# Performance work log

Measured on AMD Instinct MI355X. Metric: run time of the kernel, lower is better.

## Reference

```python
import jax, jax.numpy as jnp
import numpy as np

B, T, S, E = 32, 256, 9, 631     # batch, time, index_len, emb_num
D, FF, H, L, OUT = 512, 512, 8, 2, 512  # d_model, ffn, heads, layers, output_dim
HD = D // H
EPS = 1e-5


def _layernorm(x, g, b):
    m = jnp.mean(x, axis=-1, keepdims=True)
    v = jnp.mean(jnp.square(x - m), axis=-1, keepdims=True)
    return (x - m) * jax.lax.rsqrt(v + EPS) * g + b


def _encoder_layer(h, qkv_w, qkv_b, out_w, out_b, ln1_g, ln1_b,
                   lin1_w, lin1_b, lin2_w, lin2_b, ln2_g, ln2_b):
    # h: (N, S, D). PyTorch post-norm TransformerEncoderLayer, relu activation, dropout=0.
    N = h.shape[0]
    qkv = h @ qkv_w + qkv_b                       # (N, S, 3D)
    q, k, v = jnp.split(qkv, 3, axis=-1)
    q = q.reshape(N, S, H, HD)
    k = k.reshape(N, S, H, HD)
    v = v.reshape(N, S, H, HD)
    scores = jnp.einsum('nqhd,nkhd->nhqk', q, k) / jnp.sqrt(jnp.float32(HD))
    attn = jax.nn.softmax(scores, axis=-1)
    ctx = jnp.einsum('nhqk,nkhd->nqhd', attn, v).reshape(N, S, D)
    h = _layernorm(h + (ctx @ out_w + out_b), ln1_g, ln1_b)
    ff = jax.nn.relu(h @ lin1_w + lin1_b) @ lin2_w + lin2_b
    return _layernorm(h + ff, ln2_g, ln2_b)


def _forward(x, adapt2_w, adapt2_b, adapt_w, adapt_b,
             qkv_w, qkv_b, out_w, out_b, ln1_g, ln1_b,
             lin1_w, lin1_b, lin2_w, lin2_b, ln2_g, ln2_b, fc_w, fc_b):
    # eye_mat[x] @ W^T is a row gather: adapt_layer(onehot) == adapt_w[x] + adapt_b
    emb = adapt_w[x] + adapt_b                               # (B, T, S, D)
    # adapt_ly2(onehot.reshape(B,T,9*E)) == sum_n W2r[n, x[...,n]] + b
    w2r = adapt2_w.reshape(S, E, OUT)
    raw_emb = w2r[jnp.arange(S)[None, None, :], x].sum(axis=2) + adapt2_b  # (B, T, OUT)

    h = emb.reshape(B * T, S, D)
    for l in range(L):
        h = _encoder_layer(h, qkv_w[l], qkv_b[l], out_w[l], out_b[l],
                           ln1_g[l], ln1_b[l], lin1_w[l], lin1_b[l],
                           lin2_w[l], lin2_b[l], ln2_g[l], ln2_b[l])
    cls = h[:, 0, :]                                         # x[0] in seq-first layout
    ov = (cls @ fc_w + fc_b).reshape(B, T, OUT)
    return raw_emb * (1.0 + jax.nn.relu(ov))


def setup_inputs() -> dict:
    key = jax.random.key(0)
    ks = jax.random.split(key, 20)
    s = 0.02
    inp = {
        'x': jax.random.randint(ks[0], (B, T, S), 0, E),
        'adapt2_w': jax.random.normal(ks[1], (S * E, OUT), jnp.float32) * s,
        'adapt2_b': jnp.zeros((OUT,), jnp.float32),
        'adapt_w': jax.random.normal(ks[2], (E, D), jnp.float32) * s,
        'adapt_b': jnp.zeros((D,), jnp.float32),
        'qkv_w': jax.random.normal(ks[3], (L, D, 3 * D), jnp.float32) * s,
        'qkv_b': jnp.zeros((L, 3 * D), jnp.float32),
        'out_w': jax.random.normal(ks[4], (L, D, D), jnp.float32) * s,
        'out_b': jnp.zeros((L, D), jnp.float32),
        'ln1_g': jnp.ones((L, D), jnp.float32),
        'ln1_b': jnp.zeros((L, D), jnp.float32),
        'lin1_w': jax.random.normal(ks[5], (L, D, FF), jnp.float32) * s,
        'lin1_b': jnp.zeros((L, FF), jnp.float32),
        'lin2_w': jax.random.normal(ks[6], (L, FF, D), jnp.float32) * s,
        'lin2_b': jnp.zeros((L, D), jnp.float32),
        'ln2_g': jnp.ones((L, D), jnp.float32),
        'ln2_b': jnp.zeros((L, D), jnp.float32),
        'fc_w': jax.random.normal(ks[7], (D, OUT), jnp.float32) * s,
        'fc_b': jnp.zeros((OUT,), jnp.float32),
    }
    return inp


def reference(x, adapt2_w, adapt2_b, adapt_w, adapt_b, qkv_w, qkv_b, out_w,
              out_b, ln1_g, ln1_b, lin1_w, lin1_b, lin2_w, lin2_b, ln2_g,
              ln2_b, fc_w, fc_b):
    return _forward(x, adapt2_w, adapt2_b, adapt_w, adapt_b, qkv_w, qkv_b,
                    out_w, out_b, ln1_g, ln1_b, lin1_w, lin1_b, lin2_w,
                    lin2_b, ln2_g, ln2_b, fc_w, fc_b)
```

## Files before the change

### kernel.cpp

```cpp
#include <hip/hip_runtime.h>
#include <hip/hip_bf16.h>
#include <stdint.h>

typedef __bf16 bf16;
typedef bf16 bf16x8 __attribute__((ext_vector_type(8)));
typedef bf16 bf16x2 __attribute__((ext_vector_type(2)));
typedef float f32x4 __attribute__((ext_vector_type(4)));

__device__ __forceinline__ float b2f(bf16 x) {
  unsigned short u = __builtin_bit_cast(unsigned short, x);
  unsigned int v = ((unsigned int)u) << 16;
  return __builtin_bit_cast(float, v);
}
__device__ __forceinline__ bf16 f2b(float f) {
  unsigned int u = __builtin_bit_cast(unsigned int, f);
  unsigned int r = (u + 0x7FFFu + ((u >> 16) & 1u)) >> 16;
  return __builtin_bit_cast(bf16, (unsigned short)r);
}

__device__ __forceinline__ void async_copy16(const bf16* g, bf16* l) {
  __builtin_amdgcn_global_load_lds(
      (const __attribute__((address_space(1))) void*)g,
      (__attribute__((address_space(3))) void*)l, 16, 0, 0);
}

template <int MFR, int LDA, int LDC, int RSTR, bool RELU, bool RESID, bool RAWG, bool F32OUT, bool SWZ>
__global__ __launch_bounds__(256, (MFR == 6 ? 3 : 4)) void gemm_kernel(
    const bf16* __restrict__ A,
    const bf16* __restrict__ BT,
    const float* __restrict__ bias,
    const bf16* __restrict__ resid,
    const float* __restrict__ rawg,
    bf16* __restrict__ Cb, float* __restrict__ Cf)
{
  constexpr int K = 512;
  constexpr int MROWS = MFR * 32;
  __shared__ bf16 As[MROWS * 64];
  __shared__ bf16 Bs[128 * 64];
  const int t = threadIdx.x;
  const int lane = t & 63;
  const int wave = t >> 6;

  int bx, by;
  if (SWZ) {
    const int gn = gridDim.x, gm = gridDim.y;
    int id = blockIdx.y * gn + blockIdx.x;
    int full = (gm & ~7) * gn;
    if (id < full) {
      int sg = id / (8 * gn);
      int r = id - sg * (8 * gn);
      by = sg * 8 + (r & 7);
      bx = r >> 3;
    } else {
      int r = id - full;
      int rem = gm - (gm & ~7);
      by = (gm & ~7) + (r % rem);
      bx = r / rem;
    }
  } else {
    bx = blockIdx.x; by = blockIdx.y;
  }

  const long m0 = (long)by * MROWS;
  const int n0 = bx * 128;
  const int wm = (wave >> 1) * (MFR * 16);
  const int wn = (wave & 1) * 64;
  const int row16 = lane & 15;
  const int quad = lane >> 4;

  f32x4 acc[MFR][4] = {};

  const bf16* gA[MFR]; const bf16* gB[4];
  bf16* lA[MFR]; bf16* lB[4];
#pragma unroll
  for (int i = 0; i < MFR; i++) {
    int c = i * 256 + t;
    int row = c >> 3;
    int kc = (c & 7) ^ (row & 7);
    gA[i] = A + (m0 + row) * LDA + kc * 8;
    lA[i] = As + i * 2048 + wave * 512;
  }
#pragma unroll
  for (int i = 0; i < 4; i++) {
    int c = i * 256 + t;
    int row = c >> 3;
    int kc = (c & 7) ^ (row & 7);
    gB[i] = BT + (long)(n0 + row) * K + kc * 8;
    lB[i] = Bs + i * 2048 + wave * 512;
  }

  const int rb7 = row16 & 7;
  const bf16* paA = As + (wm + row16) * 64;
  const bf16* pbB = Bs + (wn + row16) * 64;
  const int o0 = ((0 + quad) ^ rb7) * 8;
  const int o1 = ((4 + quad) ^ rb7) * 8;

#pragma unroll 1
  for (int kt = 0; kt < K; kt += 64) {
#pragma unroll
    for (int i = 0; i < MFR; i++) async_copy16(gA[i] + kt, lA[i]);
#pragma unroll
    for (int i = 0; i < 4; i++) async_copy16(gB[i] + kt, lB[i]);
    __syncthreads();
    {
      bf16x8 af[MFR], bfr[4];
#pragma unroll
      for (int i = 0; i < MFR; i++) af[i] = *(const bf16x8*)(paA + i * 1024 + o0);
#pragma unroll
      for (int i = 0; i < 4; i++) bfr[i] = *(const bf16x8*)(pbB + i * 1024 + o0);
#pragma unroll
      for (int mi = 0; mi < MFR; mi++)
#pragma unroll
        for (int ni = 0; ni < 4; ni++)
          acc[mi][ni] = __builtin_amdgcn_mfma_f32_16x16x32_bf16(af[mi], bfr[ni], acc[mi][ni], 0, 0, 0);
    }
    {
      bf16x8 af[MFR], bfr[4];
#pragma unroll
      for (int i = 0; i < MFR; i++) af[i] = *(const bf16x8*)(paA + i * 1024 + o1);
#pragma unroll
      for (int i = 0; i < 4; i++) bfr[i] = *(const bf16x8*)(pbB + i * 1024 + o1);
#pragma unroll
      for (int mi = 0; mi < MFR; mi++)
#pragma unroll
        for (int ni = 0; ni < 4; ni++)
          acc[mi][ni] = __builtin_amdgcn_mfma_f32_16x16x32_bf16(af[mi], bfr[ni], acc[mi][ni], 0, 0, 0);
    }
    __syncthreads();
  }

  float bv[4];
#pragma unroll
  for (int ni = 0; ni < 4; ni++) bv[ni] = bias[n0 + wn + ni * 16 + row16];
#pragma unroll
  for (int mi = 0; mi < MFR; mi++) {
    long rb = m0 + wm + mi * 16 + quad * 4;
#pragma unroll
    for (int ni = 0; ni < 4; ni++) {
      int col = n0 + wn + ni * 16 + row16;
#pragma unroll
      for (int r = 0; r < 4; r++) {
        float xv = acc[mi][ni][r] + bv[ni];
        if (RESID) xv += b2f(resid[(rb + r) * RSTR + col]);
        if (RELU) xv = fmaxf(xv, 0.f);
        if (RAWG) xv = rawg[(rb + r) * 512 + col] * (1.f + fmaxf(xv, 0.f));
        if (F32OUT) Cf[(rb + r) * LDC + col] = xv;
        else        Cb[(rb + r) * LDC + col] = f2b(xv);
      }
    }
  }
}

#define ROWP 520
__global__ __launch_bounds__(512) void attn_kernel(bf16* __restrict__ qkv)
{
  __shared__ bf16 q[9 * ROWP];
  __shared__ bf16 k[9 * ROWP];
  __shared__ bf16 v[9 * ROWP];
  __shared__ float sc[8 * 81];
  const long n = blockIdx.x;
  const int t = threadIdx.x;
  bf16* base = qkv + n * (9 * 1536);
  for (int c = t; c < 1728; c += 512) {
    int o = c * 8;
    int s = o / 1536;
    int col = o - s * 1536;
    bf16x8 rawv = *(const bf16x8*)(base + o);
    bf16* dst;
    int cc;
    if (col < 512)       { dst = q; cc = col; }
    else if (col < 1024) { dst = k; cc = col - 512; }
    else                 { dst = v; cc = col - 1024; }
    *(bf16x8*)(dst + s * ROWP + cc) = rawv;
  }
  __syncthreads();
  for (int id = t; id < 648; id += 512) {
    int h = id / 81;
    int r = id - h * 81;
    int si = r / 9;
    int sj = r - si * 9;
    const bf16* qp = q + si * ROWP + h * 64;
    const bf16* kp = k + sj * ROWP + h * 64;
    float acc = 0.f;
#pragma unroll
    for (int j = 0; j < 64; j += 8) {
      bf16x8 qa = *(const bf16x8*)(qp + j);
      bf16x8 ka = *(const bf16x8*)(kp + j);
#pragma unroll
      for (int u = 0; u < 8; u++) acc += b2f(qa[u]) * b2f(ka[u]);
    }
    sc[h * 81 + si * 9 + sj] = acc * 0.125f;
  }
  __syncthreads();
  if (t < 72) {
    int h = t / 9, si = t - h * 9;
    float* row = sc + h * 81 + si * 9;
    float m = row[0];
    for (int j = 1; j < 9; j++) m = fmaxf(m, row[j]);
    float s = 0.f;
    float e[9];
    for (int j = 0; j < 9; j++) { e[j] = __expf(row[j] - m); s += e[j]; }
    float inv = 1.f / s;
    for (int j = 0; j < 9; j++) row[j] = e[j] * inv;
  }
  __syncthreads();
  for (int e2 = t; e2 < 2304; e2 += 512) {
    int si = e2 >> 8;
    int c2 = (e2 & 255) * 2;
    int h = c2 >> 6;
    const float* ar = sc + h * 81 + si * 9;
    float a0 = 0.f, a1 = 0.f;
#pragma unroll
    for (int sj = 0; sj < 9; sj++) {
      bf16x2 vv = *(const bf16x2*)(v + sj * ROWP + c2);
      float w = ar[sj];
      a0 += w * b2f(vv[0]);
      a1 += w * b2f(vv[1]);
    }
    bf16x2 o;
    o[0] = f2b(a0); o[1] = f2b(a1);
    *(bf16x2*)(base + si * 1536 + c2) = o;
  }
}

__global__ __launch_bounds__(256) void ln_kernel(const bf16* __restrict__ in, long istride,
                                                 const float* __restrict__ g, const float* __restrict__ b,
                                                 bf16* __restrict__ out, long ostride)
{
  const int t = threadIdx.x;
  const int lane = t & 63;
  const int wave = t >> 6;
  float4 g0 = *(const float4*)(g + lane * 8);
  float4 g1 = *(const float4*)(g + lane * 8 + 4);
  float4 b0 = *(const float4*)(b + lane * 8);
  float4 b1 = *(const float4*)(b + lane * 8 + 4);
  float gg[8] = {g0.x, g0.y, g0.z, g0.w, g1.x, g1.y, g1.z, g1.w};
  float bb[8] = {b0.x, b0.y, b0.z, b0.w, b1.x, b1.y, b1.z, b1.w};
#pragma unroll
  for (int r = 0; r < 2; r++) {
    const long row = ((long)blockIdx.x * 4 + wave) * 2 + r;
    const bf16* p = in + row * istride + lane * 8;
    bf16x8 xv = *(const bf16x8*)p;
    float x[8];
    float s = 0.f;
#pragma unroll
    for (int j = 0; j < 8; j++) { x[j] = b2f(xv[j]); s += x[j]; }
#pragma unroll
    for (int off = 32; off; off >>= 1) s += __shfl_xor(s, off);
    float mean = s * (1.f / 512.f);
    float vv = 0.f;
#pragma unroll
    for (int j = 0; j < 8; j++) { float d = x[j] - mean; vv += d * d; }
#pragma unroll
    for (int off = 32; off; off >>= 1) vv += __shfl_xor(vv, off);
    float inv = rsqrtf(vv * (1.f / 512.f) + 1e-5f);
    bf16x8 o;
#pragma unroll
    for (int j = 0; j < 8; j++) o[j] = f2b((x[j] - mean) * inv * gg[j] + bb[j]);
    *(bf16x8*)(out + row * ostride + lane * 8) = o;
  }
}

__global__ __launch_bounds__(256) void emb_kernel(const int* __restrict__ x, const float* __restrict__ aw,
                                                  const float* __restrict__ ab, bf16* __restrict__ h)
{
  const int t = threadIdx.x;
  const int lane = t & 63;
  const long row = (long)blockIdx.x * 4 + (t >> 6);
  const int ix = x[row];
  const float* w = aw + (long)ix * 512 + lane * 8;
  float4 w0 = *(const float4*)(w);
  float4 w1 = *(const float4*)(w + 4);
  float4 a0 = *(const float4*)(ab + lane * 8);
  float4 a1 = *(const float4*)(ab + lane * 8 + 4);
  float ww[8] = {w0.x, w0.y, w0.z, w0.w, w1.x, w1.y, w1.z, w1.w};
  float aa[8] = {a0.x, a0.y, a0.z, a0.w, a1.x, a1.y, a1.z, a1.w};
  bf16x8 o;
#pragma unroll
  for (int j = 0; j < 8; j++) o[j] = f2b(ww[j] + aa[j]);
  *(bf16x8*)(h + row * 512 + lane * 8) = o;
}

__global__ __launch_bounds__(256) void rawemb_kernel(const int* __restrict__ x, const float* __restrict__ w2,
                                                     const float* __restrict__ b2, float* __restrict__ raw)
{
  const long n = blockIdx.x;
  const int t = threadIdx.x;
  const int c = t * 2;
  float a0 = b2[c], a1 = b2[c + 1];
  for (int s = 0; s < 9; s++) {
    int ix = x[n * 9 + s];
    const float* p = w2 + ((long)(s * 631 + ix)) * 512 + c;
    a0 += p[0];
    a1 += p[1];
  }
  raw[n * 512 + c] = a0;
  raw[n * 512 + c + 1] = a1;
}

struct TP { const float* src[9]; bf16* dst[9]; int n[9]; };
__global__ __launch_bounds__(256) void transpose_kernel(TP p)
{
  const int mid = blockIdx.z;
  const int N = p.n[mid];
  if ((int)blockIdx.x * 32 >= N) return;
  const float* src = p.src[mid];
  bf16* dst = p.dst[mid];
  __shared__ float tile[32][33];
  const int tx = threadIdx.x & 31;
  const int ty0 = (threadIdx.x >> 5) * 4;
  const long kb = (long)blockIdx.y * 32, nb = (long)blockIdx.x * 32;
#pragma unroll
  for (int i = 0; i < 4; i++) tile[ty0 + i][tx] = src[(kb + ty0 + i) * N + nb + tx];
  __syncthreads();
#pragma unroll
  for (int i = 0; i < 4; i++) dst[(nb + ty0 + i) * 512 + kb + tx] = f2b(tile[tx][ty0 + i]);
}

extern "C" void kernel_launch(void* const* d_in, const int* in_sizes, int n_in,
                              void* d_out, int out_size, void* d_ws, size_t ws_size,
                              hipStream_t stream)
{
  (void)in_sizes; (void)n_in; (void)out_size;
  const int*   x        = (const int*)d_in[0];
  const float* adapt2_w = (const float*)d_in[1];
  const float* adapt2_b = (const float*)d_in[2];
  const float* adapt_w  = (const float*)d_in[3];
  const float* adapt_b  = (const float*)d_in[4];
  const float* qkv_w    = (const float*)d_in[5];
  const float* qkv_b    = (const float*)d_in[6];
  const float* out_w    = (const float*)d_in[7];
  const float* out_b    = (const float*)d_in[8];
  const float* ln1_g    = (const float*)d_in[9];
  const float* ln1_b    = (const float*)d_in[10];
  const float* lin1_w   = (const float*)d_in[11];
  const float* lin1_b   = (const float*)d_in[12];
  const float* lin2_w   = (const float*)d_in[13];
  const float* lin2_b   = (const float*)d_in[14];
  const float* ln2_g    = (const float*)d_in[15];
  const float* ln2_b    = (const float*)d_in[16];
  const float* fc_w     = (const float*)d_in[17];
  const float* fc_b     = (const float*)d_in[18];
  float* outp = (float*)d_out;
  char* ws = (char*)d_ws;

  const long wTbytes = 6815744L;
  int G = 64;
  const int cand[7] = {1, 2, 4, 8, 16, 32, 64};
  for (int i = 0; i < 7; i++) {
    long rows = 73728L / cand[i], seqs = 8192L / cand[i];
    long need = wTbytes + rows * 1024 + rows * 3072 + seqs * 2048;
    if (need <= (long)ws_size) { G = cand[i]; break; }
  }
  const long rows_c = 73728L / G;
  const long seqs_c = 8192L / G;

  bf16*  wT    = (bf16*)(ws);
  bf16*  h_c   = (bf16*)(ws + wTbytes);
  bf16*  Qc    = (bf16*)(ws + wTbytes + rows_c * 1024);
  float* raw_c = (float*)(ws + wTbytes + rows_c * 1024 + rows_c * 3072);
  bf16* qkvT  = wT;
  bf16* outT  = wT + 1572864;
  bf16* lin1T = wT + 2097152;
  bf16* lin2T = wT + 2621440;
  bf16* fcT   = wT + 3145728;

  TP tp;
  tp.src[0] = qkv_w;           tp.dst[0] = qkvT;           tp.n[0] = 1536;
  tp.src[1] = qkv_w + 786432;  tp.dst[1] = qkvT + 786432;  tp.n[1] = 1536;
  tp.src[2] = out_w;           tp.dst[2] = outT;           tp.n[2] = 512;
  tp.src[3] = out_w + 262144;  tp.dst[3] = outT + 262144;  tp.n[3] = 512;
  tp.src[4] = lin1_w;          tp.dst[4] = lin1T;          tp.n[4] = 512;
  tp.src[5] = lin1_w + 262144; tp.dst[5] = lin1T + 262144; tp.n[5] = 512;
  tp.src[6] = lin2_w;          tp.dst[6] = lin2T;          tp.n[6] = 512;
  tp.src[7] = lin2_w + 262144; tp.dst[7] = lin2T + 262144; tp.n[7] = 512;
  tp.src[8] = fc_w;            tp.dst[8] = fcT;            tp.n[8] = 512;
  hipLaunchKernelGGL(transpose_kernel, dim3(48, 16, 9), dim3(256), 0, stream, tp);

  const bf16*  nullb = nullptr;
  const float* nullf = nullptr;
  float*       nullfo = nullptr;

  for (int g = 0; g < G; g++) {
    const long row0 = (long)g * rows_c;
    const long seq0 = (long)g * seqs_c;

    hipLaunchKernelGGL(emb_kernel, dim3(rows_c / 4), dim3(256), 0, stream,
        x + row0, adapt_w, adapt_b, h_c);
    hipLaunchKernelGGL(rawemb_kernel, dim3(seqs_c), dim3(256), 0, stream,
        x + seq0 * 9, adapt2_w, adapt2_b, raw_c);

    for (int l = 0; l < 2; l++) {
      hipLaunchKernelGGL((gemm_kernel<6, 512, 1536, 1, false, false, false, false, true>),
          dim3(12, rows_c / 192), dim3(256), 0, stream,
          h_c, qkvT + l * 786432, qkv_b + l * 1536, nullb, nullf, Qc, nullfo);
      hipLaunchKernelGGL(attn_kernel, dim3(seqs_c), dim3(512), 0, stream, Qc);
      hipLaunchKernelGGL((gemm_kernel<6, 1536, 1536, 512, false, true, false, false, true>),
          dim3(4, rows_c / 192), dim3(256), 0, stream,
          Qc, outT + l * 262144, out_b + l * 512, h_c, nullf, Qc + 1024, nullfo);
      hipLaunchKernelGGL(ln_kernel, dim3(rows_c / 8), dim3(256), 0, stream,
          Qc + 1024, 1536L, ln1_g + l * 512, ln1_b + l * 512, Qc + 512, 1536L);
      hipLaunchKernelGGL((gemm_kernel<6, 1536, 1536, 1, true, false, false, false, true>),
          dim3(4, rows_c / 192), dim3(256), 0, stream,
          Qc + 512, lin1T + l * 262144, lin1_b + l * 512, nullb, nullf, Qc, nullfo);
      hipLaunchKernelGGL((gemm_kernel<6, 1536, 512, 1536, false, true, false, false, true>),
          dim3(4, rows_c / 192), dim3(256), 0, stream,
          Qc, lin2T + l * 262144, lin2_b + l * 512, Qc + 512, nullf, h_c, nullfo);
      hipLaunchKernelGGL(ln_kernel, dim3(rows_c / 8), dim3(256), 0, stream,
          h_c, 512L, ln2_g + l * 512, ln2_b + l * 512, h_c, 512L);
    }

    hipLaunchKernelGGL((gemm_kernel<4, 4608, 512, 1, false, false, true, true, false>),
        dim3(4, seqs_c / 128), dim3(256), 0, stream,
        h_c, fcT, fc_b, nullb, raw_c, (bf16*)nullptr, outp + seq0 * 512);
  }
}
```

Baseline: 1.004 ms.

## Fuse out-proj and FFN2 GEMMs with residual add and LayerNorm

Adds a gemm_ln_kernel in which each block computes a full 64x512 output row tile, then adds bias and residual, reduces row mean and variance across waves through shared memory, and writes the LayerNorm result directly. This replaces the two GEMM+separate ln_kernel pairs per layer, removing an intermediate bf16 round trip through global memory and two launches per layer. The trade-off is a large per-block B tile (512x32 staged each k-step), no double buffering, fewer and larger blocks, and single-pass variance (E[x^2]-mean^2), which is numerically less stable.

```diff
diff --git a/kernel.cpp b/kernel.cpp
--- a/kernel.cpp
+++ b/kernel.cpp
@@ -146,6 +146,120 @@
         if (RAWG) xv = rawg[(rb + r) * 512 + col] * (1.f + fmaxf(xv, 0.f));
         if (F32OUT) Cf[(rb + r) * LDC + col] = xv;
         else        Cb[(rb + r) * LDC + col] = f2b(xv);
+      }
+    }
+  }
+}
+
+template <int LDA, int RSTR, int LDC>
+__global__ __launch_bounds__(256, 2) void gemm_ln_kernel(
+    const bf16* __restrict__ A,
+    const bf16* __restrict__ BT,
+    const float* __restrict__ bias,
+    const bf16* __restrict__ resid,
+    const float* __restrict__ g,
+    const float* __restrict__ b,
+    bf16* __restrict__ C)
+{
+  constexpr int K = 512;
+  __shared__ bf16 As[64 * 32];
+  __shared__ bf16 Bs[512 * 32];
+  const int t = threadIdx.x;
+  const int lane = t & 63;
+  const int wave = t >> 6;
+  const long m0 = (long)blockIdx.x * 64;
+  const int wn = wave * 128;
+  const int row16 = lane & 15;
+  const int quad = lane >> 4;
+
+  f32x4 acc[4][8] = {};
+
+  const int rowA = t >> 2;
+  const int kcA = (t & 3) ^ ((rowA >> 1) & 3);
+  const bf16* gA = A + (m0 + rowA) * LDA + kcA * 8;
+  bf16* lA = As + wave * 512;
+  const int rB0 = t >> 2;
+  const int kcB = (t & 3) ^ ((rB0 >> 1) & 3);
+  const bf16* gB[8];
+  bf16* lB[8];
+#pragma unroll
+  for (int i = 0; i < 8; i++) {
+    gB[i] = BT + (long)(i * 64 + rB0) * K + kcB * 8;
+    lB[i] = Bs + i * 2048 + wave * 512;
+  }
+
+  const int sw = (row16 >> 1) & 3;
+  const int ofs = (quad ^ sw) * 8;
+  const bf16* pa = As + row16 * 32 + ofs;
+  const bf16* pb = Bs + (wn + row16) * 32 + ofs;
+
+#pragma unroll 1
+  for (int kt = 0; kt < K; kt += 32) {
+    async_copy16(gA + kt, lA);
+#pragma unroll
+    for (int i = 0; i < 8; i++) async_copy16(gB[i] + kt, lB[i]);
+    __syncthreads();
+    bf16x8 af[4], bfr[8];
+#pragma unroll
+    for (int i = 0; i < 4; i++) af[i] = *(const bf16x8*)(pa + i * 512);
+#pragma unroll
+    for (int i = 0; i < 8; i++) bfr[i] = *(const bf16x8*)(pb + i * 512);
+#pragma unroll
+    for (int mi = 0; mi < 4; mi++)
+#pragma unroll
+      for (int ni = 0; ni < 8; ni++)
+        acc[mi][ni] = __builtin_amdgcn_mfma_f32_16x16x32_bf16(af[mi], bfr[ni], acc[mi][ni], 0, 0, 0);
+    __syncthreads();
+  }
+
+  float bsv[8], gv[8], bvv[8];
+  int cols[8];
+#pragma unroll
+  for (int ni = 0; ni < 8; ni++) {
+    cols[ni] = wn + ni * 16 + row16;
+    bsv[ni] = bias[cols[ni]];
+    gv[ni] = g[cols[ni]];
+    bvv[ni] = b[cols[ni]];
+  }
+  float* redS = (float*)As;
+  float* redQ = redS + 256;
+#pragma unroll
+  for (int mi = 0; mi < 4; mi++) {
+#pragma unroll
+    for (int r = 0; r < 4; r++) {
+      const int lrow = mi * 16 + quad * 4 + r;
+      const long grow = m0 + lrow;
+      float s = 0.f, q = 0.f;
+#pragma unroll
+      for (int ni = 0; ni < 8; ni++) {
+        float val = acc[mi][ni][r] + bsv[ni] + b2f(resid[grow * RSTR + cols[ni]]);
+        acc[mi][ni][r] = val;
+        s += val;
+        q += val * val;
+      }
+#pragma unroll
+      for (int off = 1; off < 16; off <<= 1) {
+        s += __shfl_xor(s, off);
+        q += __shfl_xor(q, off);
+      }
+      if (row16 == 0) { redS[lrow * 4 + wave] = s; redQ[lrow * 4 + wave] = q; }
+    }
+  }
+  __syncthreads();
+#pragma unroll
+  for (int mi = 0; mi < 4; mi++) {
+#pragma unroll
+    for (int r = 0; r < 4; r++) {
+      const int lrow = mi * 16 + quad * 4 + r;
+      const long grow = m0 + lrow;
+      float S = redS[lrow * 4] + redS[lrow * 4 + 1] + redS[lrow * 4 + 2] + redS[lrow * 4 + 3];
+      float Q = redQ[lrow * 4] + redQ[lrow * 4 + 1] + redQ[lrow * 4 + 2] + redQ[lrow * 4 + 3];
+      float mean = S * (1.f / 512.f);
+      float inv = rsqrtf(Q * (1.f / 512.f) - mean * mean + 1e-5f);
+#pragma unroll
+      for (int ni = 0; ni < 8; ni++) {
+        float o = (acc[mi][ni][r] - mean) * inv * gv[ni] + bvv[ni];
+        C[grow * LDC + cols[ni]] = f2b(o);
       }
     }
   }
@@ -220,44 +334,6 @@
     bf16x2 o;
     o[0] = f2b(a0); o[1] = f2b(a1);
     *(bf16x2*)(base + si * 1536 + c2) = o;
-  }
-}
-
-__global__ __launch_bounds__(256) void ln_kernel(const bf16* __restrict__ in, long istride,
-                                                 const float* __restrict__ g, const float* __restrict__ b,
-                                                 bf16* __restrict__ out, long ostride)
-{
-  const int t = threadIdx.x;
-  const int lane = t & 63;
-  const int wave = t >> 6;
-  float4 g0 = *(const float4*)(g + lane * 8);
-  float4 g1 = *(const float4*)(g + lane * 8 + 4);
-  float4 b0 = *(const float4*)(b + lane * 8);
-  float4 b1 = *(const float4*)(b + lane * 8 + 4);
-  float gg[8] = {g0.x, g0.y, g0.z, g0.w, g1.x, g1.y, g1.z, g1.w};
-  float bb[8] = {b0.x, b0.y, b0.z, b0.w, b1.x, b1.y, b1.z, b1.w};
-#pragma unroll
-  for (int r = 0; r < 2; r++) {
-    const long row = ((long)blockIdx.x * 4 + wave) * 2 + r;
-    const bf16* p = in + row * istride + lane * 8;
-    bf16x8 xv = *(const bf16x8*)p;
-    float x[8];
-    float s = 0.f;
-#pragma unroll
-    for (int j = 0; j < 8; j++) { x[j] = b2f(xv[j]); s += x[j]; }
-#pragma unroll
-    for (int off = 32; off; off >>= 1) s += __shfl_xor(s, off);
-    float mean = s * (1.f / 512.f);
-    float vv = 0.f;
-#pragma unroll
-    for (int j = 0; j < 8; j++) { float d = x[j] - mean; vv += d * d; }
-#pragma unroll
-    for (int off = 32; off; off >>= 1) vv += __shfl_xor(vv, off);
-    float inv = rsqrtf(vv * (1.f / 512.f) + 1e-5f);
-    bf16x8 o;
-#pragma unroll
-    for (int j = 0; j < 8; j++) o[j] = f2b((x[j] - mean) * inv * gg[j] + bb[j]);
-    *(bf16x8*)(out + row * ostride + lane * 8) = o;
   }
 }
 
@@ -395,19 +471,17 @@
           dim3(12, rows_c / 192), dim3(256), 0, stream,
           h_c, qkvT + l * 786432, qkv_b + l * 1536, nullb, nullf, Qc, nullfo);
       hipLaunchKernelGGL(attn_kernel, dim3(seqs_c), dim3(512), 0, stream, Qc);
-      hipLaunchKernelGGL((gemm_kernel<6, 1536, 1536, 512, false, true, false, false, true>),
-          dim3(4, rows_c / 192), dim3(256), 0, stream,
-          Qc, outT + l * 262144, out_b + l * 512, h_c, nullf, Qc + 1024, nullfo);
-      hipLaunchKernelGGL(ln_kernel, dim3(rows_c / 8), dim3(256), 0, stream,
-          Qc + 1024, 1536L, ln1_g + l * 512, ln1_b + l * 512, Qc + 512, 1536L);
+      hipLaunchKernelGGL((gemm_ln_kernel<1536, 512, 1536>),
+          dim3(rows_c / 64), dim3(256), 0, stream,
+          Qc, outT + l * 262144, out_b + l * 512, h_c,
+          ln1_g + l * 512, ln1_b + l * 512, Qc + 512);
       hipLaunchKernelGGL((gemm_kernel<6, 1536, 1536, 1, true, false, false, false, true>),
           dim3(4, rows_c / 192), dim3(256), 0, stream,
           Qc + 512, lin1T + l * 262144, lin1_b + l * 512, nullb, nullf, Qc, nullfo);
-      hipLaunchKernelGGL((gemm_kernel<6, 1536, 512, 1536, false, true, false, false, true>),
-          dim3(4, rows_c / 192), dim3(256), 0, stream,
-          Qc, lin2T + l * 262144, lin2_b + l * 512, Qc + 512, nullf, h_c, nullfo);
-      hipLaunchKernelGGL(ln_kernel, dim3(rows_c / 8), dim3(256), 0, stream,
-          h_c, 512L, ln2_g + l * 512, ln2_b + l * 512, h_c, 512L);
+      hipLaunchKernelGGL((gemm_ln_kernel<1536, 1536, 512>),
+          dim3(rows_c / 64), dim3(256), 0, stream,
+          Qc, lin2T + l * 262144, lin2_b + l * 512, Qc + 512,
+          ln2_g + l * 512, ln2_b + l * 512, h_c);
     }
 
     hipLaunchKernelGGL((gemm_kernel<4, 4608, 512, 1, false, false, true, true, false>),
```

After: 1.143 ms. +13.9%, slower.
